# Optimization experiments

Measured on AMD Instinct MI355X. Metric: run time of the kernel, lower is better.

## Reference

```python
import jax, jax.numpy as jnp
import numpy as np

K = 9          # kernel_size
PAD = K // 2   # same padding
SIGMA = 1.0
EPS = 1e-5     # BatchNorm eps


def setup_inputs() -> dict:
    key = jax.random.key(0)
    k0, k1, k2 = jax.random.split(key, 3)
    B, Cin, Cout, L = 4, 64, 64, 131072
    x = jax.random.normal(k0, (B, Cin, L), jnp.float32)
    coords = jax.random.uniform(k1, (B, 3, L), jnp.float32)  # 3D point coords in [0,1)
    W = jax.random.normal(k2, (Cout, Cin, K), jnp.float32) * (1.0 / np.sqrt(Cin * K))
    bias = jnp.zeros((Cout,), jnp.float32)
    gamma = jnp.ones((Cout,), jnp.float32)
    beta = jnp.zeros((Cout,), jnp.float32)
    return {"x": x, "coords": coords, "W": W, "bias": bias, "gamma": gamma, "beta": beta}


def reference(x, coords, W, bias, gamma, beta):
    B, Cin, L = x.shape
    # zero-pad sequence dim for 'same' conv
    xpad = jnp.pad(x, ((0, 0), (0, 0), (PAD, PAD)))
    cpad = jnp.pad(coords, ((0, 0), (0, 0), (PAD, PAD)))
    # unfold: neighbor windows of size K (K is a small compile-time constant)
    x_unf = jnp.stack([xpad[:, :, k:k + L] for k in range(K)], axis=2)   # [B,Cin,K,L]
    c_unf = jnp.stack([cpad[:, :, k:k + L] for k in range(K)], axis=2)   # [B,3,K,L]
    # Gaussian spatial weights from coord distances (WeightedConv1D)
    dist2 = jnp.sum((c_unf - coords[:, :, None, :]) ** 2, axis=1)        # [B,K,L]
    w = jnp.exp(-dist2 / (2.0 * SIGMA * SIGMA))                          # [B,K,L]
    # weighted conv: contract over (Cin, K)
    out = jnp.einsum('ock,bckl->bol', W, x_unf * w[:, None, :, :])       # [B,Cout,L]
    out = out + bias[None, :, None]
    # BatchNorm1d (training-mode batch statistics over B and L) + ReLU
    mean = out.mean(axis=(0, 2), keepdims=True)
    var = out.var(axis=(0, 2), keepdims=True)
    out = (out - mean) * jax.lax.rsqrt(var + EPS)
    out = out * gamma[None, :, None] + beta[None, :, None]
    return jax.nn.relu(out)
```

## Files before the change

### kernel.cpp

```cpp
#include <hip/hip_runtime.h>
#include <hip/hip_bf16.h>

#define KK 9
#define PADK 4
#define CIN 64
#define COUT 64
#define LSEQ 131072
#define NB 4
#define TILEL 128
#define XROWS 136
#define XRS 72
#define NTILES 1024
#define NPART 64

typedef __attribute__((ext_vector_type(8))) short v8s;
typedef __attribute__((ext_vector_type(4))) float v4f;

__device__ __forceinline__ unsigned short f2bf(float f) {
  __hip_bfloat16 h = __float2bfloat16(f);
  return *reinterpret_cast<unsigned short*>(&h);
}
__device__ __forceinline__ float bf2f(unsigned short s) {
  return __uint_as_float(((unsigned)s) << 16);
}

__device__ __forceinline__ void store_o(float* p, float v) { *p = v; }
__device__ __forceinline__ void store_o(__hip_bfloat16* p, float v) { *p = __float2bfloat16(v); }

__global__ void wtrans_kernel(const float* __restrict__ W, v8s* __restrict__ Wt) {
  int t = blockIdx.x * 256 + threadIdx.x;
  if (t >= KK * 2 * 4 * 64) return;
  int lane = t & 63;
  int frag = t >> 6;
  int mblk = frag & 3;
  int s    = (frag >> 2) & 1;
  int k    = frag >> 3;
  int m = lane & 15, q = lane >> 4;
  int o = mblk * 16 + m;
  union { v8s v; unsigned short h[8]; } u;
#pragma unroll
  for (int j = 0; j < 8; ++j) {
    int c = 32 * s + q * 8 + j;
    u.h[j] = f2bf(W[(o * CIN + c) * KK + k]);
  }
  Wt[t] = u.v;
}

template <typename OutT>
__global__ __launch_bounds__(256, 4)
void conv_kernel(const float* __restrict__ x, const float* __restrict__ coords,
                 const v8s* __restrict__ Wt, OutT* __restrict__ cv,
                 float* __restrict__ stat_sum, float* __restrict__ stat_sq) {
  __shared__ __align__(16) __hip_bfloat16 xt[XROWS][XRS];
  __shared__ float wt[KK][TILEL];

  const int tid  = threadIdx.x;
  const int wv   = tid >> 6;
  const int wo   = wv & 1;
  const int wl   = wv >> 1;
  const int lane = tid & 63;
  const int gw   = blockIdx.x;
  const int b    = gw >> 10;
  const int tile = gw & (NTILES - 1);
  const int l0   = tile * TILEL;
  const float* xb = x + (b * CIN) * LSEQ;
  const float* cb = coords + (b * 3) * LSEQ;
  const int m = lane & 15;
  const int q = lane >> 4;

  {
    int cg = tid & 7;
    int lc = tid >> 3;
    int c8 = cg * 8;
    float4 f[8];
#pragma unroll
    for (int t = 0; t < 8; ++t)
      f[t] = *(const float4*)(xb + (c8 + t) * LSEQ + l0 + 4 * lc);
    const float* fp = (const float*)&f[0];
#pragma unroll
    for (int j = 0; j < 4; ++j) {
      union { v8s v; unsigned short h[8]; } u;
#pragma unroll
      for (int t = 0; t < 8; ++t) u.h[t] = f2bf(fp[4 * t + j]);
      *(v8s*)&xt[4 + 4 * lc + j][c8] = u.v;
    }
  }
  if (tid < 128) {
    int side = tid >> 6;
    int c = tid & 63;
    if (side == 0) {
      float el[4] = {0.f, 0.f, 0.f, 0.f};
      if (tile != 0) {
#pragma unroll
        for (int j = 0; j < 4; ++j) el[j] = xb[c * LSEQ + l0 - 4 + j];
      }
#pragma unroll
      for (int j = 0; j < 4; ++j) xt[j][c] = __float2bfloat16(el[j]);
    } else {
      float er[4] = {0.f, 0.f, 0.f, 0.f};
      if (tile != NTILES - 1) {
#pragma unroll
        for (int j = 0; j < 4; ++j) er[j] = xb[c * LSEQ + l0 + TILEL + j];
      }
#pragma unroll
      for (int j = 0; j < 4; ++j) xt[128 + 4 + j][c] = __float2bfloat16(er[j]);
    }
  }
  if (tid < TILEL) {
    int n = tid;
    float sx = cb[l0 + n];
    float sy = cb[LSEQ + l0 + n];
    float sz = cb[2 * LSEQ + l0 + n];
    float w9[KK];
#pragma unroll
    for (int k = 0; k < KK; ++k) {
      int l = l0 + n + k - PADK;
      float cx = 0.f, cy = 0.f, cz = 0.f;
      if ((unsigned)l < (unsigned)LSEQ) {
        cx = cb[l]; cy = cb[LSEQ + l]; cz = cb[2 * LSEQ + l];
      }
      float dx = cx - sx, dy = cy - sy, dz = cz - sz;
      w9[k] = __expf(-0.5f * (dx * dx + dy * dy + dz * dz));
    }
#pragma unroll
    for (int k = 0; k < KK; ++k)
      wt[k][n] = w9[k] - ((k < KK - 1) ? w9[k + 1] : 0.f);
  }
  __syncthreads();

  v4f y[2][4], tot[2][4];
#pragma unroll
  for (int i = 0; i < 2; ++i)
#pragma unroll
    for (int j = 0; j < 4; ++j) {
      y[i][j]   = (v4f){0.f, 0.f, 0.f, 0.f};
      tot[i][j] = (v4f){0.f, 0.f, 0.f, 0.f};
    }

  const v8s* wp = Wt + (wo * 2) * 64 + lane;

#pragma unroll 1
  for (int k = 0; k < KK; ++k) {
#pragma unroll
    for (int s = 0; s < 2; ++s) {
      v8s a0 = wp[k * 512 + s * 256];
      v8s a1 = wp[k * 512 + s * 256 + 64];
#pragma unroll
      for (int nbq = 0; nbq < 4; ++nbq) {
        v8s bf = *(const v8s*)&xt[wl * 64 + nbq * 16 + m + k][q * 8 + 32 * s];
        y[0][nbq] = __builtin_amdgcn_mfma_f32_16x16x32_bf16(a0, bf, y[0][nbq], 0, 0, 0);
        y[1][nbq] = __builtin_amdgcn_mfma_f32_16x16x32_bf16(a1, bf, y[1][nbq], 0, 0, 0);
      }
    }
#pragma unroll
    for (int nbq = 0; nbq < 4; ++nbq) {
      float d = wt[k][wl * 64 + nbq * 16 + m];
#pragma unroll
      for (int mb = 0; mb < 2; ++mb)
#pragma unroll
        for (int r = 0; r < 4; ++r)
          tot[mb][nbq][r] = __builtin_fmaf(d, y[mb][nbq][r], tot[mb][nbq][r]);
    }
  }

  const int part = gw & (NPART - 1);
  OutT* outb = cv + (b * COUT) * LSEQ;
#pragma unroll
  for (int mb = 0; mb < 2; ++mb) {
#pragma unroll
    for (int r = 0; r < 4; ++r) {
      int o = wo * 32 + mb * 16 + q * 4 + r;
      float s1 = 0.f, s2 = 0.f;
#pragma unroll
      for (int nbq = 0; nbq < 4; ++nbq) {
        float v = tot[mb][nbq][r];
        s1 += v;
        s2 += v * v;
        store_o(&outb[o * LSEQ + l0 + wl * 64 + nbq * 16 + m], v);
      }
#pragma unroll
      for (int off = 1; off < 16; off <<= 1) {
        s1 += __shfl_xor(s1, off, 64);
        s2 += __shfl_xor(s2, off, 64);
      }
      if (m == 0) {
        atomicAdd(&stat_sum[part * COUT + o], s1);
        atomicAdd(&stat_sq [part * COUT + o], s2);
      }
    }
  }
}

__global__ void finalize_kernel(const float* __restrict__ stat_sum,
                                const float* __restrict__ stat_sq,
                                const float* __restrict__ gamma,
                                const float* __restrict__ beta,
                                float* __restrict__ ss) {
  int o = threadIdx.x;
  float s1 = 0.f, s2 = 0.f;
  for (int p = 0; p < NPART; ++p) {
    s1 += stat_sum[p * COUT + o];
    s2 += stat_sq [p * COUT + o];
  }
  const float invN = 1.0f / (float)(NB * LSEQ);
  float mean = s1 * invN;
  float var  = s2 * invN - mean * mean;
  float sc = gamma[o] * rsqrtf(var + 1e-5f);
  ss[o]        = sc;
  ss[COUT + o] = beta[o] - mean * sc;
}

__global__ __launch_bounds__(256)
void scale_f32_kernel(float* __restrict__ data, const float* __restrict__ ss) {
  const int blk = blockIdx.x;
  const int ch = (blk >> 6) & 63;
  const float sc = ss[ch];
  const float sh = ss[COUT + ch];
  const int base = blk * 2048 + threadIdx.x * 8;
  float4 a = *(float4*)(data + base);
  float4 b = *(float4*)(data + base + 4);
  a.x = fmaxf(fmaf(a.x, sc, sh), 0.f);
  a.y = fmaxf(fmaf(a.y, sc, sh), 0.f);
  a.z = fmaxf(fmaf(a.z, sc, sh), 0.f);
  a.w = fmaxf(fmaf(a.w, sc, sh), 0.f);
  b.x = fmaxf(fmaf(b.x, sc, sh), 0.f);
  b.y = fmaxf(fmaf(b.y, sc, sh), 0.f);
  b.z = fmaxf(fmaf(b.z, sc, sh), 0.f);
  b.w = fmaxf(fmaf(b.w, sc, sh), 0.f);
  *(float4*)(data + base)     = a;
  *(float4*)(data + base + 4) = b;
}

__global__ __launch_bounds__(256)
void scale_bf16_kernel(const __hip_bfloat16* __restrict__ cvin,
                       const float* __restrict__ ss, float* __restrict__ out) {
  const int blk = blockIdx.x;
  const int ch = (blk >> 6) & 63;
  const float sc = ss[ch];
  const float sh = ss[COUT + ch];
  const int base = blk * 2048 + threadIdx.x * 8;
  union { v8s v; unsigned short h[8]; } u;
  u.v = *(const v8s*)(cvin + base);
  float r[8];
#pragma unroll
  for (int i = 0; i < 8; ++i)
    r[i] = fmaxf(fmaf(bf2f(u.h[i]), sc, sh), 0.f);
  *(float4*)(out + base)     = make_float4(r[0], r[1], r[2], r[3]);
  *(float4*)(out + base + 4) = make_float4(r[4], r[5], r[6], r[7]);
}

extern "C" void kernel_launch(void* const* d_in, const int* in_sizes, int n_in,
                              void* d_out, int out_size, void* d_ws, size_t ws_size,
                              hipStream_t stream) {
  const float* x      = (const float*)d_in[0];
  const float* coords = (const float*)d_in[1];
  const float* W      = (const float*)d_in[2];
  const float* gamma  = (const float*)d_in[4];
  const float* beta   = (const float*)d_in[5];
  float* out = (float*)d_out;
  char* ws = (char*)d_ws;

  float* stat_sum = (float*)(ws);
  float* stat_sq  = (float*)(ws + 16384);
  float* ss       = (float*)(ws + 32768);
  v8s*   Wt       = (v8s*)(ws + 40960);
  __hip_bfloat16* scratch = (__hip_bfloat16*)(ws + 131072);

  const size_t need_bf16 = (size_t)131072 + (size_t)NB * COUT * LSEQ * 2;
  const bool bf16_path = ws_size >= need_bf16;

  hipMemsetAsync(ws, 0, 32768, stream);
  wtrans_kernel<<<18, 256, 0, stream>>>(W, Wt);

  if (bf16_path) {
    conv_kernel<__hip_bfloat16><<<NB * NTILES, 256, 0, stream>>>(
        x, coords, Wt, scratch, stat_sum, stat_sq);
    finalize_kernel<<<1, COUT, 0, stream>>>(stat_sum, stat_sq, gamma, beta, ss);
    scale_bf16_kernel<<<(NB * COUT * (LSEQ / 2048)), 256, 0, stream>>>(scratch, ss, out);
  } else {
    conv_kernel<float><<<NB * NTILES, 256, 0, stream>>>(
        x, coords, Wt, out, stat_sum, stat_sq);
    finalize_kernel<<<1, COUT, 0, stream>>>(stat_sum, stat_sq, gamma, beta, ss);
    scale_f32_kernel<<<(NB * COUT * (LSEQ / 2048)), 256, 0, stream>>>(out, ss);
  }
}
```

Measured before the change: 321.0 us.

## Make conv kernel persistent with double-buffered LDS and register prefetch

The conv kernel now launches 1024 blocks, and each block loops over 4 tiles, one per batch. The next tile's x data and halo are prefetched into registers, and its Gaussian weights are computed into a second LDS buffer while the current tile's MFMA work runs. The aim is to hide global load latency behind compute and to cut block launch overhead. In exchange, register pressure rises (launch bounds drop to 3 blocks per SM), LDS use doubles, and there are fewer blocks to spread across CUs.

```diff
diff --git a/kernel.cpp b/kernel.cpp
--- a/kernel.cpp
+++ b/kernel.cpp
@@ -12,6 +12,8 @@
 #define XRS 72
 #define NTILES 1024
 #define NPART 64
+#define TPB 4
+#define NBLK 1024
 
 typedef __attribute__((ext_vector_type(8))) short v8s;
 typedef __attribute__((ext_vector_type(4))) float v4f;
@@ -47,145 +49,196 @@
 }
 
 template <typename OutT>
-__global__ __launch_bounds__(256, 4)
+__global__ __launch_bounds__(256, 3)
 void conv_kernel(const float* __restrict__ x, const float* __restrict__ coords,
                  const v8s* __restrict__ Wt, OutT* __restrict__ cv,
                  float* __restrict__ stat_sum, float* __restrict__ stat_sq) {
-  __shared__ __align__(16) __hip_bfloat16 xt[XROWS][XRS];
-  __shared__ float wt[KK][TILEL];
+  __shared__ __align__(16) __hip_bfloat16 xt[2][XROWS][XRS];
+  __shared__ float wt[2][KK][TILEL];
 
   const int tid  = threadIdx.x;
   const int wv   = tid >> 6;
   const int wo   = wv & 1;
   const int wl   = wv >> 1;
   const int lane = tid & 63;
-  const int gw   = blockIdx.x;
-  const int b    = gw >> 10;
-  const int tile = gw & (NTILES - 1);
-  const int l0   = tile * TILEL;
-  const float* xb = x + (b * CIN) * LSEQ;
-  const float* cb = coords + (b * 3) * LSEQ;
   const int m = lane & 15;
   const int q = lane >> 4;
+  const int cg = tid & 7;
+  const int lc = tid >> 3;
+  const int c8 = cg * 8;
+
+  float4 f[8];
+  float  hl[4];
 
   {
-    int cg = tid & 7;
-    int lc = tid >> 3;
-    int c8 = cg * 8;
-    float4 f[8];
+    const int gt = blockIdx.x;
+    const int b = gt >> 10, tile = gt & (NTILES - 1);
+    const int l0 = tile * TILEL;
+    const float* xb = x + (b * CIN) * LSEQ;
 #pragma unroll
     for (int t = 0; t < 8; ++t)
       f[t] = *(const float4*)(xb + (c8 + t) * LSEQ + l0 + 4 * lc);
-    const float* fp = (const float*)&f[0];
-#pragma unroll
-    for (int j = 0; j < 4; ++j) {
-      union { v8s v; unsigned short h[8]; } u;
-#pragma unroll
-      for (int t = 0; t < 8; ++t) u.h[t] = f2bf(fp[4 * t + j]);
-      *(v8s*)&xt[4 + 4 * lc + j][c8] = u.v;
-    }
-  }
-  if (tid < 128) {
-    int side = tid >> 6;
-    int c = tid & 63;
-    if (side == 0) {
-      float el[4] = {0.f, 0.f, 0.f, 0.f};
-      if (tile != 0) {
-#pragma unroll
-        for (int j = 0; j < 4; ++j) el[j] = xb[c * LSEQ + l0 - 4 + j];
-      }
-#pragma unroll
-      for (int j = 0; j < 4; ++j) xt[j][c] = __float2bfloat16(el[j]);
-    } else {
-      float er[4] = {0.f, 0.f, 0.f, 0.f};
-      if (tile != NTILES - 1) {
-#pragma unroll
-        for (int j = 0; j < 4; ++j) er[j] = xb[c * LSEQ + l0 + TILEL + j];
-      }
-#pragma unroll
-      for (int j = 0; j < 4; ++j) xt[128 + 4 + j][c] = __float2bfloat16(er[j]);
-    }
-  }
-  if (tid < TILEL) {
-    int n = tid;
-    float sx = cb[l0 + n];
-    float sy = cb[LSEQ + l0 + n];
-    float sz = cb[2 * LSEQ + l0 + n];
-    float w9[KK];
-#pragma unroll
+    if (tid < 128) {
+      int side = tid >> 6, c = tid & 63;
+      hl[0] = hl[1] = hl[2] = hl[3] = 0.f;
+      if (side == 0) {
+        if (tile != 0)
+#pragma unroll
+          for (int j = 0; j < 4; ++j) hl[j] = xb[c * LSEQ + l0 - 4 + j];
+      } else {
+        if (tile != NTILES - 1)
+#pragma unroll
+          for (int j = 0; j < 4; ++j) hl[j] = xb[c * LSEQ + l0 + TILEL + j];
+      }
+    }
+  }
+
+#pragma unroll 1
+  for (int i = 0; i < TPB; ++i) {
+    const int p  = i & 1;
+    const int gt = blockIdx.x + NBLK * i;
+    const int b = gt >> 10, tile = gt & (NTILES - 1);
+    const int l0 = tile * TILEL;
+
+    {
+      const float* fp = (const float*)&f[0];
+#pragma unroll
+      for (int j = 0; j < 4; ++j) {
+        union { v8s v; unsigned short h[8]; } u;
+#pragma unroll
+        for (int t = 0; t < 8; ++t) u.h[t] = f2bf(fp[4 * t + j]);
+        *(v8s*)&xt[p][4 + 4 * lc + j][c8] = u.v;
+      }
+    }
+    if (tid < 128) {
+      int side = tid >> 6, c = tid & 63;
+      if (side == 0) {
+#pragma unroll
+        for (int j = 0; j < 4; ++j) xt[p][j][c] = __float2bfloat16(hl[j]);
+      } else {
+#pragma unroll
+        for (int j = 0; j < 4; ++j) xt[p][132 + j][c] = __float2bfloat16(hl[j]);
+      }
+    } else if (i == 0) {
+      const float* cb = coords + (b * 3) * LSEQ;
+      int n = tid - 128;
+      float sx = cb[l0 + n], sy = cb[LSEQ + l0 + n], sz = cb[2 * LSEQ + l0 + n];
+      float w9[KK];
+#pragma unroll
+      for (int k = 0; k < KK; ++k) {
+        int l = l0 + n + k - PADK;
+        float cx = 0.f, cy = 0.f, cz = 0.f;
+        if ((unsigned)l < (unsigned)LSEQ) {
+          cx = cb[l]; cy = cb[LSEQ + l]; cz = cb[2 * LSEQ + l];
+        }
+        float dx = cx - sx, dy = cy - sy, dz = cz - sz;
+        w9[k] = __expf(-0.5f * (dx * dx + dy * dy + dz * dz));
+      }
+#pragma unroll
+      for (int k = 0; k < KK; ++k)
+        wt[p][k][n] = w9[k] - ((k < KK - 1) ? w9[k + 1] : 0.f);
+    }
+    __syncthreads();
+
+    if (i + 1 < TPB) {
+      const int gt2 = blockIdx.x + NBLK * (i + 1);
+      const int b2 = gt2 >> 10, tile2 = gt2 & (NTILES - 1);
+      const int l02 = tile2 * TILEL;
+      const float* xb2 = x + (b2 * CIN) * LSEQ;
+#pragma unroll
+      for (int t = 0; t < 8; ++t)
+        f[t] = *(const float4*)(xb2 + (c8 + t) * LSEQ + l02 + 4 * lc);
+      if (tid < 128) {
+        int side = tid >> 6, c = tid & 63;
+        hl[0] = hl[1] = hl[2] = hl[3] = 0.f;
+        if (side == 0) {
+          if (tile2 != 0)
+#pragma unroll
+            for (int j = 0; j < 4; ++j) hl[j] = xb2[c * LSEQ + l02 - 4 + j];
+        } else {
+          if (tile2 != NTILES - 1)
+#pragma unroll
+            for (int j = 0; j < 4; ++j) hl[j] = xb2[c * LSEQ + l02 + TILEL + j];
+        }
+      } else {
+        const float* cb2 = coords + (b2 * 3) * LSEQ;
+        int n = tid - 128;
+        float sx = cb2[l02 + n], sy = cb2[LSEQ + l02 + n], sz = cb2[2 * LSEQ + l02 + n];
+        float w9[KK];
+#pragma unroll
+        for (int k = 0; k < KK; ++k) {
+          int l = l02 + n + k - PADK;
+          float cx = 0.f, cy = 0.f, cz = 0.f;
+          if ((unsigned)l < (unsigned)LSEQ) {
+            cx = cb2[l]; cy = cb2[LSEQ + l]; cz = cb2[2 * LSEQ + l];
+          }
+          float dx = cx - sx, dy = cy - sy, dz = cz - sz;
+          w9[k] = __expf(-0.5f * (dx * dx + dy * dy + dz * dz));
+        }
+#pragma unroll
+        for (int k = 0; k < KK; ++k)
+          wt[p ^ 1][k][n] = w9[k] - ((k < KK - 1) ? w9[k + 1] : 0.f);
+      }
+    }
+
+    v4f y[2][4], tot[2][4];
+#pragma unroll
+    for (int a = 0; a < 2; ++a)
+#pragma unroll
+      for (int j = 0; j < 4; ++j) {
+        y[a][j]   = (v4f){0.f, 0.f, 0.f, 0.f};
+        tot[a][j] = (v4f){0.f, 0.f, 0.f, 0.f};
+      }
+
+    const v8s* wp = Wt + (wo * 2) * 64 + lane;
+#pragma unroll 1
     for (int k = 0; k < KK; ++k) {
-      int l = l0 + n + k - PADK;
-      float cx = 0.f, cy = 0.f, cz = 0.f;
-      if ((unsigned)l < (unsigned)LSEQ) {
-        cx = cb[l]; cy = cb[LSEQ + l]; cz = cb[2 * LSEQ + l];
-      }
-      float dx = cx - sx, dy = cy - sy, dz = cz - sz;
-      w9[k] = __expf(-0.5f * (dx * dx + dy * dy + dz * dz));
-    }
-#pragma unroll
-    for (int k = 0; k < KK; ++k)
-      wt[k][n] = w9[k] - ((k < KK - 1) ? w9[k + 1] : 0.f);
-  }
-  __syncthreads();
-
-  v4f y[2][4], tot[2][4];
-#pragma unroll
-  for (int i = 0; i < 2; ++i)
-#pragma unroll
-    for (int j = 0; j < 4; ++j) {
-      y[i][j]   = (v4f){0.f, 0.f, 0.f, 0.f};
-      tot[i][j] = (v4f){0.f, 0.f, 0.f, 0.f};
-    }
-
-  const v8s* wp = Wt + (wo * 2) * 64 + lane;
-
-#pragma unroll 1
-  for (int k = 0; k < KK; ++k) {
-#pragma unroll
-    for (int s = 0; s < 2; ++s) {
-      v8s a0 = wp[k * 512 + s * 256];
-      v8s a1 = wp[k * 512 + s * 256 + 64];
+#pragma unroll
+      for (int s = 0; s < 2; ++s) {
+        v8s a0 = wp[k * 512 + s * 256];
+        v8s a1 = wp[k * 512 + s * 256 + 64];
+#pragma unroll
+        for (int nbq = 0; nbq < 4; ++nbq) {
+          v8s bf = *(const v8s*)&xt[p][wl * 64 + nbq * 16 + m + k][q * 8 + 32 * s];
+          y[0][nbq] = __builtin_amdgcn_mfma_f32_16x16x32_bf16(a0, bf, y[0][nbq], 0, 0, 0);
+          y[1][nbq] = __builtin_amdgcn_mfma_f32_16x16x32_bf16(a1, bf, y[1][nbq], 0, 0, 0);
+        }
+      }
 #pragma unroll
       for (int nbq = 0; nbq < 4; ++nbq) {
-        v8s bf = *(const v8s*)&xt[wl * 64 + nbq * 16 + m + k][q * 8 + 32 * s];
-        y[0][nbq] = __builtin_amdgcn_mfma_f32_16x16x32_bf16(a0, bf, y[0][nbq], 0, 0, 0);
-        y[1][nbq] = __builtin_amdgcn_mfma_f32_16x16x32_bf16(a1, bf, y[1][nbq], 0, 0, 0);
-      }
-    }
-#pragma unroll
-    for (int nbq = 0; nbq < 4; ++nbq) {
-      float d = wt[k][wl * 64 + nbq * 16 + m];
-#pragma unroll
-      for (int mb = 0; mb < 2; ++mb)
-#pragma unroll
-        for (int r = 0; r < 4; ++r)
-          tot[mb][nbq][r] = __builtin_fmaf(d, y[mb][nbq][r], tot[mb][nbq][r]);
-    }
-  }
-
-  const int part = gw & (NPART - 1);
-  OutT* outb = cv + (b * COUT) * LSEQ;
-#pragma unroll
-  for (int mb = 0; mb < 2; ++mb) {
-#pragma unroll
-    for (int r = 0; r < 4; ++r) {
-      int o = wo * 32 + mb * 16 + q * 4 + r;
-      float s1 = 0.f, s2 = 0.f;
-#pragma unroll
-      for (int nbq = 0; nbq < 4; ++nbq) {
-        float v = tot[mb][nbq][r];
-        s1 += v;
-        s2 += v * v;
-        store_o(&outb[o * LSEQ + l0 + wl * 64 + nbq * 16 + m], v);
-      }
-#pragma unroll
-      for (int off = 1; off < 16; off <<= 1) {
-        s1 += __shfl_xor(s1, off, 64);
-        s2 += __shfl_xor(s2, off, 64);
-      }
-      if (m == 0) {
-        atomicAdd(&stat_sum[part * COUT + o], s1);
-        atomicAdd(&stat_sq [part * COUT + o], s2);
+        float d = wt[p][k][wl * 64 + nbq * 16 + m];
+#pragma unroll
+        for (int mb = 0; mb < 2; ++mb)
+#pragma unroll
+          for (int r = 0; r < 4; ++r)
+            tot[mb][nbq][r] = __builtin_fmaf(d, y[mb][nbq][r], tot[mb][nbq][r]);
+      }
+    }
+
+    const int part = gt & (NPART - 1);
+    OutT* outb = cv + (b * COUT) * LSEQ;
+#pragma unroll
+    for (int mb = 0; mb < 2; ++mb) {
+#pragma unroll
+      for (int r = 0; r < 4; ++r) {
+        int o = wo * 32 + mb * 16 + q * 4 + r;
+        float s1 = 0.f, s2 = 0.f;
+#pragma unroll
+        for (int nbq = 0; nbq < 4; ++nbq) {
+          float v = tot[mb][nbq][r];
+          s1 += v;
+          s2 += v * v;
+          store_o(&outb[o * LSEQ + l0 + wl * 64 + nbq * 16 + m], v);
+        }
+#pragma unroll
+        for (int off = 1; off < 16; off <<= 1) {
+          s1 += __shfl_xor(s1, off, 64);
+          s2 += __shfl_xor(s2, off, 64);
+        }
+        if (m == 0) {
+          atomicAdd(&stat_sum[part * COUT + o], s1);
+          atomicAdd(&stat_sq [part * COUT + o], s2);
+        }
       }
     }
   }
@@ -273,12 +326,12 @@
   wtrans_kernel<<<18, 256, 0, stream>>>(W, Wt);
 
   if (bf16_path) {
-    conv_kernel<__hip_bfloat16><<<NB * NTILES, 256, 0, stream>>>(
+    conv_kernel<__hip_bfloat16><<<NBLK, 256, 0, stream>>>(
         x, coords, Wt, scratch, stat_sum, stat_sq);
     finalize_kernel<<<1, COUT, 0, stream>>>(stat_sum, stat_sq, gamma, beta, ss);
     scale_bf16_kernel<<<(NB * COUT * (LSEQ / 2048)), 256, 0, stream>>>(scratch, ss, out);
   } else {
-    conv_kernel<float><<<NB * NTILES, 256, 0, stream>>>(
+    conv_kernel<float><<<NBLK, 256, 0, stream>>>(
         x, coords, Wt, out, stat_sum, stat_sq);
     finalize_kernel<<<1, COUT, 0, stream>>>(stat_sum, stat_sq, gamma, beta, ss);
     scale_f32_kernel<<<(NB * COUT * (LSEQ / 2048)), 256, 0, stream>>>(out, ss);
```

New measurement: 384.3 us. 19.7% more time.
